# Kernel optimization log

Hardware: AMD Instinct MI355X
Metric: run time of the kernel (lower is better)

## Reference

```python
import jax, jax.numpy as jnp
import numpy as np

B, C, H, W = 16, 256, 32, 32
N_E, E_DIM = 8192, 256
BETA = 0.25
ENT_RATIO = 0.1
TEMP = 0.01


def _normalize(x, eps=1e-6):
    # torch F.normalize: x / clamp_min(||x||, eps)
    n = jnp.linalg.norm(x, axis=-1, keepdims=True)
    return x / jnp.maximum(n, eps)


def setup_inputs() -> dict:
    key = jax.random.key(0)
    k1, k2, k3 = jax.random.split(key, 3)
    z = jax.random.normal(k1, (B, C, H, W), dtype=jnp.float32)
    # nn.Embedding init: normal(0, e_dim**-0.5)
    emb_weight = jax.random.normal(k2, (N_E, E_DIM), dtype=jnp.float32) * (E_DIM ** -0.5)
    # nn.Linear(e_dim, e_dim)
    proj_w = jax.random.normal(k3, (E_DIM, E_DIM), dtype=jnp.float32) * (E_DIM ** -0.5)
    proj_b = jnp.zeros((E_DIM,), dtype=jnp.float32)
    return {"z": z, "emb_weight": emb_weight, "proj_w": proj_w, "proj_b": proj_b}


def reference(z, emb_weight, proj_w, proj_b):
    sg = jax.lax.stop_gradient
    # SimVQ: project the (frozen) codebook through a linear layer
    weight = emb_weight @ proj_w.T + proj_b            # [K, d]
    b, c, h, w = z.shape
    z_bhwc = jnp.transpose(z, (0, 2, 3, 1))            # [B,H,W,C]
    z_flat = z_bhwc.reshape(b, h * w, c)               # [B,L,C]

    # l2_norm=True branch
    zn = _normalize(z_flat)                             # [B,L,d]
    wn = _normalize(weight)                             # [K,d]

    z2 = jnp.sum(zn * zn, axis=-1, keepdims=True)       # [B,L,1]
    w2 = jnp.sum(wn * wn, axis=-1)[None, None, :]       # [1,1,K]
    dot = jnp.einsum('bld,kd->blk', zn, wn)             # [B,L,K]
    dists = z2 + w2 - 2.0 * dot                         # [B,L,K]

    indices = jnp.argmin(dists, axis=-1)                # [B,L]
    q = wn[indices].reshape(b, h, w, c)                 # gather normalized codebook

    # training losses (l2_norm=True -> compare normalized)
    z_cmp = _normalize(z_bhwc)
    q_cmp = _normalize(q)
    codebook_loss = jnp.mean((q_cmp - sg(z_cmp)) ** 2)
    commit_loss = BETA * jnp.mean((sg(q_cmp) - z_cmp) ** 2)

    # entropy loss on affinity = -dists
    a = (-dists).reshape(-1, dists.shape[-1]) / TEMP    # [B*L, K]
    probs = jax.nn.softmax(a, axis=-1)
    log_probs = jax.nn.log_softmax(a + 1e-5, axis=-1)
    avg_probs = jnp.mean(probs, axis=0)
    avg_entropy = -jnp.sum(avg_probs * jnp.log(avg_probs + 1e-5))
    sample_entropy = -jnp.mean(jnp.sum(probs * log_probs, axis=-1))
    entropy_loss = ENT_RATIO * (sample_entropy - avg_entropy)

    # straight-through estimator, back to channel-first
    z_q = z_bhwc + sg(q - z_bhwc)
    z_q = jnp.transpose(z_q, (0, 3, 1, 2))              # [B,C,H,W]
    flat_indices = indices.reshape(-1)
    return (z_q, codebook_loss, commit_loss, entropy_loss, flat_indices)
```

## Files before the change

kernel.cpp:

```cpp
#include <hip/hip_runtime.h>
#include <math.h>

#define NROWS 16384
#define NCODES 8192
#define DIMS 256
#define NCS 4
#define CEXP 288.5390082f

#define OFF_WN   0u
#define OFF_W2   2097152u
#define OFF_ZN   2105344u
#define OFF_WNH  6299648u
#define OFF_WNL  7348224u
#define OFF_ZNH  8396800u
#define OFF_ZNL  10493952u
#define OFF_PL1  12591104u
#define OFF_PL2  12656640u
#define OFF_PS   12722176u
#define OFF_PI1  12787712u
#define OFF_PI2  12853248u
#define OFF_RM   12918784u
#define OFF_RS   12935168u
#define OFF_RIDX 12951552u
#define OFF_AVGP 12967936u
#define OFF_SCAL 12976128u

typedef __attribute__((ext_vector_type(8))) short bf16x8;
typedef __attribute__((ext_vector_type(4))) float f32x4;
typedef unsigned short u16;

__device__ __forceinline__ u16 f2bf(float f) {
  unsigned u = __float_as_uint(f);
  u += 0x7fffu + ((u >> 16) & 1u);
  return (u16)(u >> 16);
}
__device__ __forceinline__ float bf2f(u16 s) { return __uint_as_float(((unsigned)s) << 16); }

__device__ __forceinline__ void gl_lds16(const u16* g, u16* l) {
  __builtin_amdgcn_global_load_lds(
      (const __attribute__((address_space(1))) unsigned*)g,
      (__attribute__((address_space(3))) unsigned*)l, 16, 0, 0);
}

#define PHASE_BARRIER_CNT()  asm volatile("s_waitcnt vmcnt(4) lgkmcnt(0)\n\ts_barrier" ::: "memory")
#define PHASE_BARRIER_ALL()  asm volatile("s_waitcnt vmcnt(0) lgkmcnt(0)\n\ts_barrier" ::: "memory")
#define LGKM_BARRIER()       asm volatile("s_waitcnt lgkmcnt(0)\n\ts_barrier" ::: "memory")
#define DRAIN_VM()           asm volatile("s_waitcnt vmcnt(0)" ::: "memory")

__device__ __forceinline__ void ins2(float x, int idx, float& b1, int& i1, float& b2, int& i2) {
  if (x > b1 || (x == b1 && idx < i1)) { b2 = b1; i2 = i1; b1 = x; i1 = idx; }
  else if (x > b2 || (x == b2 && idx < i2)) { b2 = x; i2 = idx; }
}

__global__ __launch_bounds__(256) void k0_init(float* ws) {
  int i = blockIdx.x * 256 + threadIdx.x;
  if (i < NCODES) ws[OFF_AVGP + i] = 0.f;
  if (i < 16) ws[OFF_SCAL + i] = 0.f;
}

__global__ __launch_bounds__(256) void k1_codebook(const float* __restrict__ emb,
    const float* __restrict__ pw, const float* __restrict__ pb,
    float* __restrict__ wn, float* __restrict__ w2,
    u16* __restrict__ wnh, u16* __restrict__ wnl) {
  __shared__ float e[256];
  __shared__ float red[256];
  int k = blockIdx.x, t = threadIdx.x;
  e[t] = emb[(size_t)k * 256 + t];
  __syncthreads();
  const float4* prow = reinterpret_cast<const float4*>(pw + (size_t)t * 256);
  float acc = pb[t];
  #pragma unroll 8
  for (int q = 0; q < 64; ++q) {
    float4 p4 = prow[q];
    acc += e[q*4+0]*p4.x + e[q*4+1]*p4.y + e[q*4+2]*p4.z + e[q*4+3]*p4.w;
  }
  red[t] = acc * acc;
  __syncthreads();
  for (int s = 128; s; s >>= 1) { if (t < s) red[t] += red[t+s]; __syncthreads(); }
  float inv = 1.f / fmaxf(sqrtf(red[0]), 1e-6f);
  float v = acc * inv;
  size_t o = (size_t)k*256 + t;
  wn[o] = v;
  u16 hb = f2bf(v); float hf = bf2f(hb);
  wnh[o] = hb; wnl[o] = f2bf(v - hf);
  __syncthreads();
  red[t] = v * v;
  __syncthreads();
  for (int s = 128; s; s >>= 1) { if (t < s) red[t] += red[t+s]; __syncthreads(); }
  if (t == 0) w2[k] = red[0];
}

__global__ __launch_bounds__(256) void k2_zn(const float* __restrict__ z,
    float* __restrict__ zn, u16* __restrict__ znh, u16* __restrict__ znl) {
  __shared__ float tile[256][33];
  __shared__ float inv[32];
  int bh = blockIdx.x, t = threadIdx.x;
  const float* zb = z + (size_t)(bh >> 5) * (256*1024) + (size_t)(bh & 31) * 32;
  for (int j = 0; j < 32; ++j) {
    int i = t + j*256; int c = i >> 5, w = i & 31;
    tile[c][w] = zb[(size_t)c*1024 + w];
  }
  __syncthreads();
  if (t < 32) {
    float s = 0.f;
    for (int c = 0; c < 256; ++c) { float v = tile[c][t]; s += v*v; }
    inv[t] = 1.f / fmaxf(sqrtf(s), 1e-6f);
  }
  __syncthreads();
  size_t base = (size_t)bh * 32 * 256;
  for (int w = 0; w < 32; ++w) {
    float v = tile[t][w] * inv[w];
    size_t o = base + (size_t)w*256 + t;
    zn[o] = v;
    u16 hb = f2bf(v); float hf = bf2f(hb);
    znh[o] = hb; znl[o] = f2bf(v - hf);
  }
}

__global__ __attribute__((amdgpu_flat_work_group_size(256,256)))
__attribute__((amdgpu_waves_per_eu(2,4))) void k3_pass1(
    const u16* __restrict__ znh, const u16* __restrict__ znl,
    const u16* __restrict__ wnh, const u16* __restrict__ wnl,
    float* __restrict__ pL1, float* __restrict__ pL2, float* __restrict__ pS,
    int* __restrict__ pI1, int* __restrict__ pI2) {
  __shared__ u16 Cbuf[3][2][128*32];
  __shared__ float mrgF[2][2][32][3];
  __shared__ int   mrgI[2][2][32][2];
  int t = threadIdx.x;
  int rb = blockIdx.x >> 2, cs = blockIdx.x & 3;
  int r0 = rb * 64;
  int w = t >> 6, l = t & 63;
  int wxc = w & 1, wy = w >> 1;
  int g = l >> 4, lr = l & 15;

  bf16x8 bh[2][8], bl[2][8];
  #pragma unroll
  for (int jr = 0; jr < 2; ++jr) {
    size_t rbase = (size_t)(r0 + wy*32 + jr*16 + lr) * 256;
    #pragma unroll
    for (int dc = 0; dc < 8; ++dc) {
      bh[jr][dc] = *(const bf16x8*)&znh[rbase + dc*32 + g*8];
      bl[jr][dc] = *(const bf16x8*)&znl[rbase + dc*32 + g*8];
    }
  }

  const size_t csbase = (size_t)cs * 2048 * 256;
  auto stage = [&](int s, int b) {
    int dc2 = s & 7;
    int krow = (s >> 3) * 128;
    #pragma unroll
    for (int rnd = 0; rnd < 2; ++rnd) {
      int i = rnd*256 + t;
      int code = i >> 2, q = i & 3;
      size_t go = csbase + (size_t)(krow + code)*256 + dc2*32 + q*8;
      gl_lds16(&wnh[go], &Cbuf[b][0][rnd*2048 + w*512]);
      gl_lds16(&wnl[go], &Cbuf[b][1][rnd*2048 + w*512]);
    }
  };
  DRAIN_VM();
  stage(0, 0);
  stage(1, 1);

  float b1[2] = {-3.0e38f, -3.0e38f}, b2[2] = {-3.0e38f, -3.0e38f}, Sv[2] = {0.f, 0.f};
  int i1[2] = {0, 0}, i2[2] = {0, 0};

  for (int kt = 0; kt < 16; ++kt) {
    f32x4 acc[4][2];
    #pragma unroll
    for (int i = 0; i < 4; ++i) { acc[i][0] = (f32x4){0.f,0.f,0.f,0.f}; acc[i][1] = (f32x4){0.f,0.f,0.f,0.f}; }
    #pragma unroll
    for (int dc = 0; dc < 8; ++dc) {
      int s = kt*8 + dc;
      if (s < 127) PHASE_BARRIER_CNT(); else PHASE_BARRIER_ALL();
      if (s + 2 < 128) {
        int bS = s + 2; bS -= (bS/3)*3;
        stage(s + 2, bS);
      }
      int bR = s - (s/3)*3;
      #pragma unroll
      for (int i = 0; i < 4; ++i) {
        int co = (wxc*64 + i*16 + lr)*32 + g*8;
        bf16x8 ah = *(const bf16x8*)&Cbuf[bR][0][co];
        bf16x8 al = *(const bf16x8*)&Cbuf[bR][1][co];
        acc[i][0] = __builtin_amdgcn_mfma_f32_16x16x32_bf16(ah, bh[0][dc], acc[i][0], 0, 0, 0);
        acc[i][1] = __builtin_amdgcn_mfma_f32_16x16x32_bf16(ah, bh[1][dc], acc[i][1], 0, 0, 0);
        acc[i][0] = __builtin_amdgcn_mfma_f32_16x16x32_bf16(ah, bl[0][dc], acc[i][0], 0, 0, 0);
        acc[i][1] = __builtin_amdgcn_mfma_f32_16x16x32_bf16(ah, bl[1][dc], acc[i][1], 0, 0, 0);
        acc[i][0] = __builtin_amdgcn_mfma_f32_16x16x32_bf16(al, bh[0][dc], acc[i][0], 0, 0, 0);
        acc[i][1] = __builtin_amdgcn_mfma_f32_16x16x32_bf16(al, bh[1][dc], acc[i][1], 0, 0, 0);
      }
    }
    int kb16 = kt * 16;
    #pragma unroll
    for (int jr = 0; jr < 2; ++jr) {
      float xv[16];
      #pragma unroll
      for (int n = 0; n < 16; ++n) xv[n] = acc[n>>2][jr][n&3];
      float ob1 = b1[jr];
      #pragma unroll
      for (int n = 0; n < 16; ++n) {
        float x = xv[n];
        bool c1 = x > b1[jr];
        bool c2 = x > b2[jr];
        float hi = fmaxf(x, b1[jr]);
        float lo = fminf(x, b1[jr]);
        b2[jr] = fmaxf(lo, fminf(hi, b2[jr]));
        i2[jr] = c1 ? i1[jr] : (c2 ? (kb16 + n) : i2[jr]);
        b1[jr] = hi;
        i1[jr] = c1 ? (kb16 + n) : i1[jr];
      }
      float negCm = -CEXP * b1[jr];
      float ts0 = 0.f, ts1 = 0.f;
      #pragma unroll
      for (int n = 0; n < 16; n += 2) {
        ts0 += exp2f(fmaf(CEXP, xv[n],   negCm));
        ts1 += exp2f(fmaf(CEXP, xv[n+1], negCm));
      }
      Sv[jr] = Sv[jr] * exp2f(CEXP * (ob1 - b1[jr])) + (ts0 + ts1);
    }
  }
  float my[2], y2[2]; int gi1[2], gi2[2];
  #pragma unroll
  for (int jr = 0; jr < 2; ++jr) {
    int e1 = i1[jr], e2 = i2[jr];
    int base = cs*2048 + wxc*64 + g*4;
    gi1[jr] = base + (e1>>4)*128 + ((e1&15)>>2)*16 + (e1&3);
    gi2[jr] = base + (e2>>4)*128 + ((e2&15)>>2)*16 + (e2&3);
    my[jr] = CEXP * b1[jr];
    y2[jr] = CEXP * b2[jr];
    #pragma unroll
    for (int mask = 16; mask <= 32; mask <<= 1) {
      float om  = __shfl_xor(my[jr], mask, 64);
      float oy2 = __shfl_xor(y2[jr], mask, 64);
      float oS  = __shfl_xor(Sv[jr], mask, 64);
      int   o1  = __shfl_xor(gi1[jr], mask, 64);
      int   o2  = __shfl_xor(gi2[jr], mask, 64);
      float pm = my[jr];
      ins2(om,  o1, my[jr], gi1[jr], y2[jr], gi2[jr]);
      ins2(oy2, o2, my[jr], gi1[jr], y2[jr], gi2[jr]);
      Sv[jr] = Sv[jr] * exp2f(pm - my[jr]) + oS * exp2f(om - my[jr]);
    }
  }
  __syncthreads();
  if (g == 0) {
    #pragma unroll
    for (int jr = 0; jr < 2; ++jr) {
      int ri = jr*16 + lr;
      mrgF[wy][wxc][ri][0] = my[jr]; mrgF[wy][wxc][ri][1] = y2[jr]; mrgF[wy][wxc][ri][2] = Sv[jr];
      mrgI[wy][wxc][ri][0] = gi1[jr]; mrgI[wy][wxc][ri][1] = gi2[jr];
    }
  }
  __syncthreads();
  if (t < 64) {
    int wyy = t >> 5, ri = t & 31;
    float m1 = mrgF[wyy][0][ri][0], m2 = mrgF[wyy][0][ri][1], S = mrgF[wyy][0][ri][2];
    int a1 = mrgI[wyy][0][ri][0], a2 = mrgI[wyy][0][ri][1];
    float om1 = mrgF[wyy][1][ri][0], om2 = mrgF[wyy][1][ri][1], oS = mrgF[wyy][1][ri][2];
    int ob1i = mrgI[wyy][1][ri][0], ob2i = mrgI[wyy][1][ri][1];
    float pm = m1;
    ins2(om1, ob1i, m1, a1, m2, a2);
    ins2(om2, ob2i, m1, a1, m2, a2);
    S = S * exp2f(pm - m1) + oS * exp2f(om1 - m1);
    int r = r0 + wyy*32 + ri;
    size_t o = (size_t)cs * NROWS + r;
    pL1[o] = m1; pL2[o] = m2; pS[o] = S;
    pI1[o] = a1; pI2[o] = a2;
  }
}

__global__ __launch_bounds__(256) void k3b_refine(
    const float* __restrict__ zn, const float* __restrict__ wn, const float* __restrict__ w2,
    const float* __restrict__ pL1, const float* __restrict__ pL2, const float* __restrict__ pS,
    const int* __restrict__ pI1, const int* __restrict__ pI2,
    float* __restrict__ rm, float* __restrict__ rs, int* __restrict__ ridx) {
  int t = threadIdx.x;
  int r = blockIdx.x * 4 + (t >> 6);
  int l = t & 63;
  float b1 = pL1[r], b2 = pL2[r], S = pS[r];
  int i1 = pI1[r], i2 = pI2[r];
  #pragma unroll
  for (int c = 1; c < NCS; ++c) {
    size_t o = (size_t)c * NROWS + r;
    float ob1 = pL1[o], ob2 = pL2[o], oS = pS[o];
    int oi1 = pI1[o], oi2 = pI2[o];
    float pb1 = b1;
    ins2(ob1, oi1, b1, i1, b2, i2);
    ins2(ob2, oi2, b1, i1, b2, i2);
    S = S * exp2f(pb1 - b1) + oS * exp2f(ob1 - b1);
  }
  int cand = (l < 32) ? i1 : i2;
  int lo = l & 31;
  const float* zr = zn + (size_t)r * 256;
  const float* wc = wn + (size_t)cand * 256;
  float d = 0.f;
  #pragma unroll
  for (int q = 0; q < 8; ++q) d += zr[lo + q*32] * wc[lo + q*32];
  #pragma unroll
  for (int mask = 1; mask <= 16; mask <<= 1) d += __shfl_xor(d, mask, 64);
  float dOther = __shfl_xor(d, 32, 64);
  if (l == 0) {
    float s1 = w2[i1] - 2.f*d;
    float s2 = w2[i2] - 2.f*dOther;
    int win = i1;
    if (s2 < s1 || (s2 == s1 && i2 < i1)) win = i2;
    rm[r] = b1; rs[r] = S; ridx[r] = win;
  }
}

__global__ __attribute__((amdgpu_flat_work_group_size(256,256)))
__attribute__((amdgpu_waves_per_eu(2,4))) void k4_pass2(
    const u16* __restrict__ znh, const u16* __restrict__ znl,
    const u16* __restrict__ wnh, const u16* __restrict__ wnl,
    const float* __restrict__ rm, const float* __restrict__ rs,
    float* __restrict__ avgp, float* __restrict__ scal) {
  __shared__ u16 Cbuf[3][2][128*32];
  __shared__ float avgLds[2][128];
  __shared__ float red[256];
  int t = threadIdx.x;
  int rb = blockIdx.x >> 2, cs = blockIdx.x & 3;
  int r0 = rb * 64;
  int w = t >> 6, l = t & 63;
  int wxc = w & 1, wy = w >> 1;
  int g = l >> 4, lr = l & 15;

  bf16x8 bh[2][8], bl[2][8];
  #pragma unroll
  for (int jr = 0; jr < 2; ++jr) {
    size_t rbase = (size_t)(r0 + wy*32 + jr*16 + lr) * 256;
    #pragma unroll
    for (int dc = 0; dc < 8; ++dc) {
      bh[jr][dc] = *(const bf16x8*)&znh[rbase + dc*32 + g*8];
      bl[jr][dc] = *(const bf16x8*)&znl[rbase + dc*32 + g*8];
    }
  }
  float m_[2], invS[2], l2s[2];
  #pragma unroll
  for (int jr = 0; jr < 2; ++jr) {
    int r = r0 + wy*32 + jr*16 + lr;
    float mm = rm[r], ss = rs[r];
    m_[jr] = mm; invS[jr] = 1.f / ss; l2s[jr] = log2f(ss);
  }

  const size_t csbase = (size_t)cs * 2048 * 256;
  auto stage = [&](int s, int b) {
    int dc2 = s & 7;
    int krow = (s >> 3) * 128;
    #pragma unroll
    for (int rnd = 0; rnd < 2; ++rnd) {
      int i = rnd*256 + t;
      int code = i >> 2, q = i & 3;
      size_t go = csbase + (size_t)(krow + code)*256 + dc2*32 + q*8;
      gl_lds16(&wnh[go], &Cbuf[b][0][rnd*2048 + w*512]);
      gl_lds16(&wnl[go], &Cbuf[b][1][rnd*2048 + w*512]);
    }
  };
  DRAIN_VM();
  stage(0, 0);
  stage(1, 1);
  float ent = 0.f;

  for (int kt = 0; kt < 16; ++kt) {
    f32x4 acc[4][2];
    #pragma unroll
    for (int i = 0; i < 4; ++i) { acc[i][0] = (f32x4){0.f,0.f,0.f,0.f}; acc[i][1] = (f32x4){0.f,0.f,0.f,0.f}; }
    #pragma unroll
    for (int dc = 0; dc < 8; ++dc) {
      int s = kt*8 + dc;
      if (s < 127) PHASE_BARRIER_CNT(); else PHASE_BARRIER_ALL();
      if (s + 2 < 128) {
        int bS = s + 2; bS -= (bS/3)*3;
        stage(s + 2, bS);
      }
      int bR = s - (s/3)*3;
      #pragma unroll
      for (int i = 0; i < 4; ++i) {
        int co = (wxc*64 + i*16 + lr)*32 + g*8;
        bf16x8 ah = *(const bf16x8*)&Cbuf[bR][0][co];
        bf16x8 al = *(const bf16x8*)&Cbuf[bR][1][co];
        acc[i][0] = __builtin_amdgcn_mfma_f32_16x16x32_bf16(ah, bh[0][dc], acc[i][0], 0, 0, 0);
        acc[i][1] = __builtin_amdgcn_mfma_f32_16x16x32_bf16(ah, bh[1][dc], acc[i][1], 0, 0, 0);
        acc[i][0] = __builtin_amdgcn_mfma_f32_16x16x32_bf16(ah, bl[0][dc], acc[i][0], 0, 0, 0);
        acc[i][1] = __builtin_amdgcn_mfma_f32_16x16x32_bf16(ah, bl[1][dc], acc[i][1], 0, 0, 0);
        acc[i][0] = __builtin_amdgcn_mfma_f32_16x16x32_bf16(al, bh[0][dc], acc[i][0], 0, 0, 0);
        acc[i][1] = __builtin_amdgcn_mfma_f32_16x16x32_bf16(al, bh[1][dc], acc[i][1], 0, 0, 0);
      }
    }
    int kb = cs*2048 + kt*128;
    float codeAcc[16];
    #pragma unroll
    for (int n = 0; n < 16; ++n) codeAcc[n] = 0.f;
    #pragma unroll
    for (int jr = 0; jr < 2; ++jr) {
      float m = m_[jr], is = invS[jr], l2 = l2s[jr];
      #pragma unroll
      for (int i = 0; i < 4; ++i)
        #pragma unroll
        for (int v = 0; v < 4; ++v) {
          float tt = fmaf(CEXP, acc[i][jr][v], -m);
          float p = exp2f(tt) * is;
          ent -= p * (tt - l2);
          codeAcc[i*4+v] += p;
        }
    }
    #pragma unroll
    for (int n = 0; n < 16; ++n) {
      float s = codeAcc[n];
      s += __shfl_xor(s, 1, 64);
      s += __shfl_xor(s, 2, 64);
      s += __shfl_xor(s, 4, 64);
      s += __shfl_xor(s, 8, 64);
      if (lr == 0) avgLds[wy][wxc*64 + (n>>2)*16 + g*4 + (n&3)] = s;
    }
    LGKM_BARRIER();
    if (t < 128) atomicAdd(&avgp[kb + t], (avgLds[0][t] + avgLds[1][t]) * (1.f/16384.f));
  }
  red[t] = ent;
  __syncthreads();
  for (int s2 = 128; s2; s2 >>= 1) { if (t < s2) red[t] += red[t + s2]; __syncthreads(); }
  if (t == 0) atomicAdd(&scal[1], red[0] * 0.6931471806f);
}

__global__ __launch_bounds__(256) void k5_gather(const float* __restrict__ zn,
    const float* __restrict__ wn, const int* __restrict__ row_idx,
    float* __restrict__ out_zq, float* __restrict__ scal) {
  __shared__ float tile[256][33];
  __shared__ float red4[4];
  __shared__ float red[256];
  int bh = blockIdx.x, t = threadIdx.x;
  int b = bh >> 5, h = bh & 31;
  float cb = 0.f;
  for (int w = 0; w < 32; ++w) {
    int r = bh*32 + w;
    int idx = row_idx[r];
    float q = wn[(size_t)idx*256 + t];
    float s = q*q;
    #pragma unroll
    for (int mask = 32; mask; mask >>= 1) s += __shfl_xor(s, mask, 64);
    if ((t & 63) == 0) red4[t >> 6] = s;
    __syncthreads();
    float tot = red4[0] + red4[1] + red4[2] + red4[3];
    float inv = 1.f / fmaxf(sqrtf(tot), 1e-6f);
    float zv = zn[(size_t)r*256 + t];
    float d = q*inv - zv;
    cb += d*d;
    tile[t][w] = q;
    __syncthreads();
  }
  red[t] = cb;
  __syncthreads();
  for (int s2 = 128; s2; s2 >>= 1) { if (t < s2) red[t] += red[t+s2]; __syncthreads(); }
  if (t == 0) atomicAdd(&scal[0], red[0]);
  float* ob = out_zq + (size_t)b*256*1024 + (size_t)h*32;
  for (int j = 0; j < 32; ++j) {
    int i = t + j*256; int c = i >> 5, ww = i & 31;
    ob[(size_t)c*1024 + ww] = tile[c][ww];
  }
}

__global__ __launch_bounds__(256) void k6_final(const float* __restrict__ avg_probs,
    const float* __restrict__ scal, const int* __restrict__ row_idx,
    float* __restrict__ out) {
  int t = threadIdx.x;
  if (blockIdx.x < 64) {
    int r = blockIdx.x*256 + t;
    out[4194307 + r] = (float)row_idx[r];
    return;
  }
  __shared__ float red[256];
  float s = 0.f;
  for (int j = 0; j < 32; ++j) {
    float v = avg_probs[t + j*256];
    s -= v * logf(v + 1e-5f);
  }
  red[t] = s;
  __syncthreads();
  for (int q = 128; q; q >>= 1) { if (t < q) red[t] += red[t+q]; __syncthreads(); }
  if (t == 0) {
    float avg_entropy = red[0];
    float sample_entropy = scal[1] * (1.f/16384.f);
    float cb = scal[0] * (1.f/4194304.f);
    out[4194304] = cb;
    out[4194305] = 0.25f * cb;
    out[4194306] = 0.1f * (sample_entropy - avg_entropy);
  }
}

extern "C" void kernel_launch(void* const* d_in, const int* in_sizes, int n_in,
                              void* d_out, int out_size, void* d_ws, size_t ws_size,
                              hipStream_t stream) {
  const float* z   = (const float*)d_in[0];
  const float* emb = (const float*)d_in[1];
  const float* pw  = (const float*)d_in[2];
  const float* pb  = (const float*)d_in[3];
  float* ws  = (float*)d_ws;
  float* out = (float*)d_out;
  float* wn   = ws + OFF_WN;
  float* w2   = ws + OFF_W2;
  float* zn   = ws + OFF_ZN;
  u16*   wnh  = (u16*)(ws + OFF_WNH);
  u16*   wnl  = (u16*)(ws + OFF_WNL);
  u16*   znh  = (u16*)(ws + OFF_ZNH);
  u16*   znl  = (u16*)(ws + OFF_ZNL);
  float* pL1  = ws + OFF_PL1;
  float* pL2  = ws + OFF_PL2;
  float* pS   = ws + OFF_PS;
  int*   pI1  = (int*)(ws + OFF_PI1);
  int*   pI2  = (int*)(ws + OFF_PI2);
  float* rm   = ws + OFF_RM;
  float* rs   = ws + OFF_RS;
  int*   ridx = (int*)(ws + OFF_RIDX);
  float* avgp = ws + OFF_AVGP;
  float* scal = ws + OFF_SCAL;

  k0_init<<<32, 256, 0, stream>>>(ws);
  k1_codebook<<<NCODES, 256, 0, stream>>>(emb, pw, pb, wn, w2, wnh, wnl);
  k2_zn<<<512, 256, 0, stream>>>(z, zn, znh, znl);
  k3_pass1<<<1024, 256, 0, stream>>>(znh, znl, wnh, wnl, pL1, pL2, pS, pI1, pI2);
  k3b_refine<<<NROWS/4, 256, 0, stream>>>(zn, wn, w2, pL1, pL2, pS, pI1, pI2, rm, rs, ridx);
  k4_pass2<<<1024, 256, 0, stream>>>(znh, znl, wnh, wnl, rm, rs, avgp, scal);
  k5_gather<<<512, 256, 0, stream>>>(zn, wn, ridx, out, scal);
  k6_final<<<65, 256, 0, stream>>>(avgp, scal, ridx, out);
}
```

Before: 858.6 us.

## Give each wave a private codebook LDS buffer to drop block barriers

In both GEMM passes, each wave now stages only its own 64-code slice into a private double-buffered LDS region. The per-stage block-wide s_barrier is replaced by per-wave vmcnt and lgkmcnt waits, so waves no longer synchronise with each other in the main loop. Pass 2 also drops the LDS cross-wave reduction of average probabilities and barrier in favour of direct per-lane global atomics. The trade-off is that the two waves sharing a code slice (wy=0,1) now each load the same codebook data, doubling global/L2 traffic for that data. Pass 2 also issues more atomics per tile.

```diff
diff --git a/kernel.cpp b/kernel.cpp
--- a/kernel.cpp
+++ b/kernel.cpp
@@ -42,10 +42,10 @@
       (__attribute__((address_space(3))) unsigned*)l, 16, 0, 0);
 }
 
-#define PHASE_BARRIER_CNT()  asm volatile("s_waitcnt vmcnt(4) lgkmcnt(0)\n\ts_barrier" ::: "memory")
-#define PHASE_BARRIER_ALL()  asm volatile("s_waitcnt vmcnt(0) lgkmcnt(0)\n\ts_barrier" ::: "memory")
-#define LGKM_BARRIER()       asm volatile("s_waitcnt lgkmcnt(0)\n\ts_barrier" ::: "memory")
-#define DRAIN_VM()           asm volatile("s_waitcnt vmcnt(0)" ::: "memory")
+#define WAIT_VM8()   asm volatile("s_waitcnt vmcnt(8)" ::: "memory")
+#define WAIT_VM24()  asm volatile("s_waitcnt vmcnt(24)" ::: "memory")
+#define DRAIN_VM()   asm volatile("s_waitcnt vmcnt(0)" ::: "memory")
+#define LGKM_DRAIN() asm volatile("s_waitcnt lgkmcnt(0)" ::: "memory")
 
 __device__ __forceinline__ void ins2(float x, int idx, float& b1, int& i1, float& b2, int& i2) {
   if (x > b1 || (x == b1 && idx < i1)) { b2 = b1; i2 = i1; b1 = x; i1 = idx; }
@@ -123,7 +123,7 @@
     const u16* __restrict__ wnh, const u16* __restrict__ wnl,
     float* __restrict__ pL1, float* __restrict__ pL2, float* __restrict__ pS,
     int* __restrict__ pI1, int* __restrict__ pI2) {
-  __shared__ u16 Cbuf[3][2][128*32];
+  __shared__ u16 Cbuf[4][2][2][2048];
   __shared__ float mrgF[2][2][32][3];
   __shared__ int   mrgI[2][2][32][2];
   int t = threadIdx.x;
@@ -149,12 +149,11 @@
     int dc2 = s & 7;
     int krow = (s >> 3) * 128;
     #pragma unroll
-    for (int rnd = 0; rnd < 2; ++rnd) {
-      int i = rnd*256 + t;
-      int code = i >> 2, q = i & 3;
-      size_t go = csbase + (size_t)(krow + code)*256 + dc2*32 + q*8;
-      gl_lds16(&wnh[go], &Cbuf[b][0][rnd*2048 + w*512]);
-      gl_lds16(&wnl[go], &Cbuf[b][1][rnd*2048 + w*512]);
+    for (int j = 0; j < 4; ++j) {
+      int cl = j*16 + (l >> 2);
+      size_t go = csbase + (size_t)(krow + wxc*64 + cl)*256 + dc2*32 + (l & 3)*8;
+      gl_lds16(&wnh[go], &Cbuf[w][b][0][j*512]);
+      gl_lds16(&wnl[go], &Cbuf[w][b][1][j*512]);
     }
   };
   DRAIN_VM();
@@ -171,17 +170,13 @@
     #pragma unroll
     for (int dc = 0; dc < 8; ++dc) {
       int s = kt*8 + dc;
-      if (s < 127) PHASE_BARRIER_CNT(); else PHASE_BARRIER_ALL();
-      if (s + 2 < 128) {
-        int bS = s + 2; bS -= (bS/3)*3;
-        stage(s + 2, bS);
-      }
-      int bR = s - (s/3)*3;
+      if (s < 127) WAIT_VM8(); else DRAIN_VM();
+      int bR = s & 1;
       #pragma unroll
       for (int i = 0; i < 4; ++i) {
-        int co = (wxc*64 + i*16 + lr)*32 + g*8;
-        bf16x8 ah = *(const bf16x8*)&Cbuf[bR][0][co];
-        bf16x8 al = *(const bf16x8*)&Cbuf[bR][1][co];
+        int co = (i*16 + lr)*32 + g*8;
+        bf16x8 ah = *(const bf16x8*)&Cbuf[w][bR][0][co];
+        bf16x8 al = *(const bf16x8*)&Cbuf[w][bR][1][co];
         acc[i][0] = __builtin_amdgcn_mfma_f32_16x16x32_bf16(ah, bh[0][dc], acc[i][0], 0, 0, 0);
         acc[i][1] = __builtin_amdgcn_mfma_f32_16x16x32_bf16(ah, bh[1][dc], acc[i][1], 0, 0, 0);
         acc[i][0] = __builtin_amdgcn_mfma_f32_16x16x32_bf16(ah, bl[0][dc], acc[i][0], 0, 0, 0);
@@ -189,6 +184,8 @@
         acc[i][0] = __builtin_amdgcn_mfma_f32_16x16x32_bf16(al, bh[0][dc], acc[i][0], 0, 0, 0);
         acc[i][1] = __builtin_amdgcn_mfma_f32_16x16x32_bf16(al, bh[1][dc], acc[i][1], 0, 0, 0);
       }
+      LGKM_DRAIN();
+      if (s + 2 < 128) stage(s + 2, bR);
     }
     int kb16 = kt * 16;
     #pragma unroll
@@ -313,8 +310,7 @@
     const u16* __restrict__ wnh, const u16* __restrict__ wnl,
     const float* __restrict__ rm, const float* __restrict__ rs,
     float* __restrict__ avgp, float* __restrict__ scal) {
-  __shared__ u16 Cbuf[3][2][128*32];
-  __shared__ float avgLds[2][128];
+  __shared__ u16 Cbuf[4][2][2][2048];
   __shared__ float red[256];
   int t = threadIdx.x;
   int rb = blockIdx.x >> 2, cs = blockIdx.x & 3;
@@ -346,12 +342,11 @@
     int dc2 = s & 7;
     int krow = (s >> 3) * 128;
     #pragma unroll
-    for (int rnd = 0; rnd < 2; ++rnd) {
-      int i = rnd*256 + t;
-      int code = i >> 2, q = i & 3;
-      size_t go = csbase + (size_t)(krow + code)*256 + dc2*32 + q*8;
-      gl_lds16(&wnh[go], &Cbuf[b][0][rnd*2048 + w*512]);
-      gl_lds16(&wnl[go], &Cbuf[b][1][rnd*2048 + w*512]);
+    for (int j = 0; j < 4; ++j) {
+      int cl = j*16 + (l >> 2);
+      size_t go = csbase + (size_t)(krow + wxc*64 + cl)*256 + dc2*32 + (l & 3)*8;
+      gl_lds16(&wnh[go], &Cbuf[w][b][0][j*512]);
+      gl_lds16(&wnl[go], &Cbuf[w][b][1][j*512]);
     }
   };
   DRAIN_VM();
@@ -366,17 +361,15 @@
     #pragma unroll
     for (int dc = 0; dc < 8; ++dc) {
       int s = kt*8 + dc;
-      if (s < 127) PHASE_BARRIER_CNT(); else PHASE_BARRIER_ALL();
-      if (s + 2 < 128) {
-        int bS = s + 2; bS -= (bS/3)*3;
-        stage(s + 2, bS);
-      }
-      int bR = s - (s/3)*3;
+      if (s == 127) { DRAIN_VM(); }
+      else if (dc == 0 && kt > 0) { WAIT_VM24(); }
+      else { WAIT_VM8(); }
+      int bR = s & 1;
       #pragma unroll
       for (int i = 0; i < 4; ++i) {
-        int co = (wxc*64 + i*16 + lr)*32 + g*8;
-        bf16x8 ah = *(const bf16x8*)&Cbuf[bR][0][co];
-        bf16x8 al = *(const bf16x8*)&Cbuf[bR][1][co];
+        int co = (i*16 + lr)*32 + g*8;
+        bf16x8 ah = *(const bf16x8*)&Cbuf[w][bR][0][co];
+        bf16x8 al = *(const bf16x8*)&Cbuf[w][bR][1][co];
         acc[i][0] = __builtin_amdgcn_mfma_f32_16x16x32_bf16(ah, bh[0][dc], acc[i][0], 0, 0, 0);
         acc[i][1] = __builtin_amdgcn_mfma_f32_16x16x32_bf16(ah, bh[1][dc], acc[i][1], 0, 0, 0);
         acc[i][0] = __builtin_amdgcn_mfma_f32_16x16x32_bf16(ah, bl[0][dc], acc[i][0], 0, 0, 0);
@@ -384,6 +377,8 @@
         acc[i][0] = __builtin_amdgcn_mfma_f32_16x16x32_bf16(al, bh[0][dc], acc[i][0], 0, 0, 0);
         acc[i][1] = __builtin_amdgcn_mfma_f32_16x16x32_bf16(al, bh[1][dc], acc[i][1], 0, 0, 0);
       }
+      LGKM_DRAIN();
+      if (s + 2 < 128) stage(s + 2, bR);
     }
     int kb = cs*2048 + kt*128;
     float codeAcc[16];
@@ -404,15 +399,14 @@
     }
     #pragma unroll
     for (int n = 0; n < 16; ++n) {
-      float s = codeAcc[n];
-      s += __shfl_xor(s, 1, 64);
-      s += __shfl_xor(s, 2, 64);
-      s += __shfl_xor(s, 4, 64);
-      s += __shfl_xor(s, 8, 64);
-      if (lr == 0) avgLds[wy][wxc*64 + (n>>2)*16 + g*4 + (n&3)] = s;
-    }
-    LGKM_BARRIER();
-    if (t < 128) atomicAdd(&avgp[kb + t], (avgLds[0][t] + avgLds[1][t]) * (1.f/16384.f));
+      float sv = codeAcc[n];
+      sv += __shfl_xor(sv, 1, 64);
+      sv += __shfl_xor(sv, 2, 64);
+      sv += __shfl_xor(sv, 4, 64);
+      sv += __shfl_xor(sv, 8, 64);
+      if (lr == 0)
+        atomicAdd(&avgp[kb + wxc*64 + (n>>2)*16 + g*4 + (n&3)], sv * (1.f/16384.f));
+    }
   }
   red[t] = ent;
   __syncthreads();
```

Measured after the change: 1.156 ms. 1.35x slower.
